# Optimization experiments

Hardware: AMD Instinct MI355X
Metric: run time of the kernel (lower is better)

## Reference

```python
import jax, jax.numpy as jnp
import numpy as np

N, E, C_IN, HID, K, NLAYERS = 1024, 2048, 4, 192, 5, 4


def setup_inputs() -> dict:
    key = jax.random.key(0)
    ks = jax.random.split(key, 24)
    s = 0.05
    x = jax.random.normal(ks[0], (N, C_IN), jnp.float32)
    src = jax.random.randint(ks[1], (E,), 0, N, dtype=jnp.int32)
    off = jax.random.randint(ks[2], (E,), 1, N, dtype=jnp.int32)
    dst = (src + off) % N  # guarantees no self-loops (ChebConv removes them)
    edge_index = jnp.stack([src, dst])  # [2, E] int32
    edge_attr = jax.random.normal(ks[3], (E, C_IN), jnp.float32)
    batch = jnp.zeros((N,), jnp.int32)  # unused by forward, kept for signature fidelity
    inp = {
        'x': x, 'edge_index': edge_index, 'edge_attr': edge_attr, 'batch': batch,
        # ChebConv(4, 192, K=5): K weight mats + bias
        'cheb_w': jax.random.normal(ks[4], (K, C_IN, HID), jnp.float32) * s,
        'cheb_b': jnp.zeros((HID,), jnp.float32),
        # edge encoder Linear(4, 192)
        'eenc_w': jax.random.normal(ks[5], (C_IN, HID), jnp.float32) * s,
        'eenc_b': jnp.zeros((HID,), jnp.float32),
        # 4 NNConv layers, each with MapE2NxN edge MLP (192->192->192*192),
        # root linear (192x192, no bias) and conv bias
        'nn1_w': jax.random.normal(ks[6], (NLAYERS, HID, HID), jnp.float32) * s,
        'nn1_b': jnp.zeros((NLAYERS, HID), jnp.float32),
        'nn2_w': jax.random.normal(ks[7], (NLAYERS, HID, HID * HID), jnp.float32) * (s / 8.0),
        'nn2_b': jnp.zeros((NLAYERS, HID * HID), jnp.float32),
        'root_w': jax.random.normal(ks[8], (NLAYERS, HID, HID), jnp.float32) * s,
        'conv_b': jnp.zeros((NLAYERS, HID), jnp.float32),
        # LayerNorm per DeepGCNLayer
        'ln_g': jnp.ones((NLAYERS, HID), jnp.float32),
        'ln_b': jnp.zeros((NLAYERS, HID), jnp.float32),
        # final Linear(192, 2)
        'out_w': jax.random.normal(ks[9], (HID, 2), jnp.float32) * s,
        'out_b': jnp.zeros((2,), jnp.float32),
    }
    return inp


def _layernorm(v, g, b):
    mu = jnp.mean(v, axis=-1, keepdims=True)
    var = jnp.mean(jnp.square(v - mu), axis=-1, keepdims=True)
    return (v - mu) * jax.lax.rsqrt(var + 1e-5) * g + b


def reference(x, edge_index, edge_attr, batch, cheb_w, cheb_b, eenc_w, eenc_b,
              nn1_w, nn1_b, nn2_w, nn2_b, root_w, conv_b, ln_g, ln_b, out_w, out_b):
    n = x.shape[0]
    src, dst = edge_index[0], edge_index[1]

    # ---- ChebConv (sym norm, lambda_max=2.0) => L_hat = -D^{-1/2} A D^{-1/2} ----
    deg = jax.ops.segment_sum(jnp.ones_like(src, dtype=x.dtype), src, num_segments=n)
    dinv = jnp.where(deg > 0, 1.0 / jnp.sqrt(jnp.maximum(deg, 1.0)), 0.0)
    wnorm = -dinv[src] * dinv[dst]  # [E]

    def lap(v):  # y = L_hat @ v : gather -> weight -> scatter-add
        return jax.ops.segment_sum(wnorm[:, None] * v[src], dst, num_segments=n)

    Tx0 = x
    out = Tx0 @ cheb_w[0]
    Tx1 = lap(Tx0)
    out = out + Tx1 @ cheb_w[1]
    for k in range(2, K):  # Chebyshev recurrence
        Tx2 = 2.0 * lap(Tx1) - Tx0
        out = out + Tx2 @ cheb_w[k]
        Tx0, Tx1 = Tx1, Tx2
    h = out + cheb_b  # [N, HID]

    # ---- edge encoder ----
    ea = edge_attr @ eenc_w + eenc_b  # [E, HID]

    # ---- NNConv: per-edge MLP-generated weight, gather->edge-GEMM->scatter ----
    def nnconv(v, i):
        theta = (ea @ nn1_w[i] + nn1_b[i]) @ nn2_w[i] + nn2_b[i]  # [E, HID*HID]
        theta = theta.reshape(E, HID, HID)
        msg = jnp.einsum('ei,eio->eo', v[src], theta)  # per-edge matvec
        agg = jax.ops.segment_sum(msg, dst, num_segments=n)  # aggr='add'
        return agg + v @ root_w[i] + conv_b[i]

    # layers[0].conv applied directly (no pre-norm/act)
    h = nnconv(h, 0)
    # layers[1:4] are DeepGCNLayer res+: x + conv(dropout(act(norm(x))))
    for i in range(1, NLAYERS):
        z = jax.nn.relu(_layernorm(h, ln_g[i], ln_b[i]))
        h = h + nnconv(z, i)
    # final: act(layers[0].norm(x)), dropout (eval=identity), linear
    h = jax.nn.relu(_layernorm(h, ln_g[0], ln_b[0]))
    return h @ out_w + out_b  # [N, 2]
```

## Files before the change

### kernel.cpp

```cpp
#include <hip/hip_runtime.h>
#include <stdint.h>

typedef _Float16 half8 __attribute__((ext_vector_type(8)));
typedef float f32x4 __attribute__((ext_vector_type(4)));

typedef const __attribute__((address_space(1))) void* gptr_t;
typedef __attribute__((address_space(3))) void* lptr_t;
static __device__ __forceinline__ void gll16(const void* g, void* l) {
  __builtin_amdgcn_global_load_lds((gptr_t)(unsigned long long)g,
                                   (lptr_t)(unsigned int)(unsigned long long)l,
                                   16, 0, 0);
}

__global__ __launch_bounds__(256)
void k_pb(const float* __restrict__ nn2_w, const float* __restrict__ nn2_b,
          const float* __restrict__ eenc_w, const float* __restrict__ eenc_b,
          const float* __restrict__ nn1_w, const float* __restrict__ nn1_b,
          const float* __restrict__ root_w, _Float16* __restrict__ Btl,
          const float* __restrict__ x, const int* __restrict__ ei,
          float* __restrict__ Tx, int* __restrict__ rowptr, int* __restrict__ eord) {
  __shared__ __align__(16) float smem[33728];
  int t = threadIdx.x;
  if (blockIdx.x >= 36) {
    if (blockIdx.x == 36) {
      if (blockIdx.y == 0) {
        float* cur = smem;
        float* yv = smem + 4096;
        float* deg = yv;
        for (int i = t; i < 1024; i += 256) deg[i] = 0.f;
        __syncthreads();
        for (int e = t; e < 2048; e += 256) atomicAdd(&deg[ei[e]], 1.f);
        __syncthreads();
        float wn[8];
#pragma unroll
        for (int i = 0; i < 8; ++i) {
          int e = t + 256 * i;
          int s = ei[e], d = ei[2048 + e];
          float ds = deg[s], dd = deg[d];
          float a = ds > 0.f ? 1.f / sqrtf(fmaxf(ds, 1.f)) : 0.f;
          float bb = dd > 0.f ? 1.f / sqrtf(fmaxf(dd, 1.f)) : 0.f;
          wn[i] = -a * bb;
        }
        __syncthreads();
        float4 prev[4];
#pragma unroll
        for (int q = 0; q < 4; ++q) {
          int i = t + 256 * q;
          float4 xv = ((const float4*)x)[i];
          ((float4*)cur)[i] = xv;
          ((float4*)Tx)[i] = xv;
        }
        __syncthreads();
        for (int rec = 0; rec < 4; ++rec) {
          for (int i = t; i < 4096; i += 256) yv[i] = 0.f;
          __syncthreads();
#pragma unroll
          for (int i = 0; i < 8; ++i) {
            int e = t + 256 * i;
            int s = ei[e], d = ei[2048 + e];
            float wv = wn[i];
#pragma unroll
            for (int c = 0; c < 4; ++c) atomicAdd(&yv[d * 4 + c], wv * cur[s * 4 + c]);
          }
          __syncthreads();
          float a = rec ? 2.f : 1.f;
#pragma unroll
          for (int q = 0; q < 4; ++q) {
            int i = t + 256 * q;
            float4 y4 = ((float4*)yv)[i];
            float4 c4 = ((float4*)cur)[i];
            float4 n4;
            n4.x = a * y4.x - (rec ? prev[q].x : 0.f);
            n4.y = a * y4.y - (rec ? prev[q].y : 0.f);
            n4.z = a * y4.z - (rec ? prev[q].z : 0.f);
            n4.w = a * y4.w - (rec ? prev[q].w : 0.f);
            prev[q] = c4;
            ((float4*)cur)[i] = n4;
            ((float4*)(Tx + (rec + 1) * 4096))[i] = n4;
          }
          __syncthreads();
        }
      } else if (blockIdx.y == 1) {
        int* cnt = (int*)smem;
        int* rp  = (int*)smem + 1024;
        int* wtot = (int*)smem + 2048;
        int lane = t & 63, wv = t >> 6;
        for (int i = t; i < 1024; i += 256) cnt[i] = 0;
        __syncthreads();
        for (int e = t; e < 2048; e += 256) atomicAdd(&cnt[ei[2048 + e]], 1);
        __syncthreads();
        int c0 = cnt[t * 4], c1 = cnt[t * 4 + 1], c2 = cnt[t * 4 + 2], c3 = cnt[t * 4 + 3];
        int s = c0 + c1 + c2 + c3;
        int inc = s;
#pragma unroll
        for (int off = 1; off < 64; off <<= 1) {
          int u = __shfl_up(inc, off);
          if (lane >= off) inc += u;
        }
        if (lane == 63) wtot[wv] = inc;
        __syncthreads();
        int woff = 0;
#pragma unroll
        for (int j = 0; j < 4; ++j) if (j < wv) woff += wtot[j];
        int excl = woff + inc - s;
        int4 r4; r4.x = excl; r4.y = excl + c0; r4.z = excl + c0 + c1; r4.w = excl + c0 + c1 + c2;
        *(int4*)(rowptr + t * 4) = r4;
        if (t == 0) rowptr[1024] = 2048;
        rp[t * 4] = r4.x; rp[t * 4 + 1] = r4.y; rp[t * 4 + 2] = r4.z; rp[t * 4 + 3] = r4.w;
        __syncthreads();
        for (int e = t; e < 2048; e += 256) {
          int d = ei[2048 + e];
          int slot = atomicAdd(&rp[d], 1);
          eord[slot] = e;
        }
      }
      return;
    }
    int l = blockIdx.y;
    for (int idx = t; idx < 36864; idx += 256) {
      float v = root_w[(size_t)l * 36864 + idx];
      int i = idx / 192, o = idx - i * 192;
      Btl[(size_t)l * 221184 + (i >> 3) * 9216 + (size_t)(960 + o) * 8 + (i & 7)] = (_Float16)v;
    }
    return;
  }
  int w = t >> 6, lane = t & 63;
  int l = blockIdx.y;
  int wcol = blockIdx.x * 1024 + w * 256;
  const float* W2l = nn2_w + (size_t)l * 7077888;
  char* ldsbase = (char*)smem + w * 32768;
  f32x4 nb4 = *(const f32x4*)(nn2_b + (size_t)l * 36864 + wcol + 4 * lane);

#define ISSUE(tile)                                                             \
  {                                                                             \
    _Pragma("unroll")                                                           \
    for (int r = 0; r < 4; ++r) {                                               \
      int row = (tile) * 4 + r;                                                 \
      gll16((const char*)(W2l + (size_t)row * 36864 + wcol) + lane * 16,        \
            ldsbase + ((tile) & 7) * 4096 + r * 1024 + lane * 16);              \
    }                                                                           \
  }

  ISSUE(0); ISSUE(1); ISSUE(2); ISSUE(3); ISSUE(4); ISSUE(5); ISSUE(6);
  if (t < 192) {
    float a0 = 0.f, a1 = 0.f, a2 = 0.f, a3 = 0.f, a4 = 0.f;
    const float* nw = nn1_w + (size_t)l * 36864 + t;
    for (int k = 0; k < 192; ++k) {
      float nv = nw[(size_t)k * 192];
      a0 += eenc_w[k] * nv;
      a1 += eenc_w[192 + k] * nv;
      a2 += eenc_w[384 + k] * nv;
      a3 += eenc_w[576 + k] * nv;
      a4 += eenc_b[k] * nv;
    }
    smem[32768 + t] = a0; smem[32960 + t] = a1; smem[33152 + t] = a2;
    smem[33344 + t] = a3; smem[33536 + t] = a4 + nn1_b[l * 192 + t];
  }
  __syncthreads();

  f32x4 a[5] = {};
  const float* Ms = smem + 32768;
  for (int tile = 0; tile < 48; ++tile) {
    if (tile < 41) ISSUE(tile + 7);
    if (tile < 41)       asm volatile("s_waitcnt vmcnt(28)" ::: "memory");
    else if (tile == 41) asm volatile("s_waitcnt vmcnt(24)" ::: "memory");
    else if (tile == 42) asm volatile("s_waitcnt vmcnt(20)" ::: "memory");
    else if (tile == 43) asm volatile("s_waitcnt vmcnt(16)" ::: "memory");
    else if (tile == 44) asm volatile("s_waitcnt vmcnt(12)" ::: "memory");
    else if (tile == 45) asm volatile("s_waitcnt vmcnt(8)" ::: "memory");
    else if (tile == 46) asm volatile("s_waitcnt vmcnt(4)" ::: "memory");
    else                 asm volatile("s_waitcnt vmcnt(0)" ::: "memory");
    const float* wb = (const float*)(ldsbase) + (tile & 7) * 1024;
    const float* Mt = Ms + tile * 4;
#pragma unroll
    for (int r = 0; r < 4; ++r) {
      f32x4 wv = *(const f32x4*)(wb + r * 256 + 4 * lane);
#pragma unroll
      for (int c = 0; c < 5; ++c) a[c] += Mt[c * 192 + r] * wv;
    }
  }
#undef ISSUE
  a[4] += nb4;
#pragma unroll
  for (int cc = 0; cc < 4; ++cc) {
    int col = wcol + 4 * lane + cc;
    int i = col / 192, o = col - i * 192;
    _Float16* B0 = Btl + (size_t)l * 221184 + (i >> 3) * 9216 + (i & 7);
#pragma unroll
    for (int c = 0; c < 5; ++c)
      B0[(size_t)(c * 192 + o) * 8] = (_Float16)a[c][cc];
  }
}

__global__ __launch_bounds__(256)
void k_y(const _Float16* __restrict__ z16, const _Float16* __restrict__ Btl,
         float* __restrict__ Y, const float* __restrict__ Tx,
         const float* __restrict__ cheb_w, const float* __restrict__ cheb_b, int layer) {
  __shared__ __align__(16) _Float16 Als[12288];
  int t = threadIdx.x;
  int w = t >> 6, lane = t & 63, l15 = lane & 15, q4 = lane >> 4;
  int e0 = blockIdx.x * 64, cb = blockIdx.y;
  if (layer == 0) {
#pragma unroll
    for (int it = 0; it < 6; ++it) {
      int u = it * 256 + t;
      int row = u & 63, ck = u >> 6;
      int n = e0 + row;
      float tv[5][4];
#pragma unroll
      for (int k = 0; k < 5; ++k) {
        float4 t4 = ((const float4*)(Tx + k * 4096))[n];
        tv[k][0] = t4.x; tv[k][1] = t4.y; tv[k][2] = t4.z; tv[k][3] = t4.w;
      }
      union { _Float16 h[8]; uint4 v; } u8;
#pragma unroll
      for (int j = 0; j < 8; ++j) {
        int o = ck * 8 + j;
        float acc = cheb_b[o];
#pragma unroll
        for (int k = 0; k < 5; ++k)
#pragma unroll
          for (int c = 0; c < 4; ++c)
            acc += tv[k][c] * cheb_w[(k * 4 + c) * 192 + o];
        u8.h[j] = (_Float16)acc;
      }
      *(uint4*)(Als + (size_t)u * 8) = u8.v;
    }
    __syncthreads();
  }
  const _Float16* Bt = Btl + (size_t)layer * 221184;
  const _Float16* ap = z16 + (((size_t)q4 * 1024) + e0 + w * 16 + l15) * 8;
  const _Float16* bp = Bt + (((size_t)q4 * 1152) + cb * 192 + l15) * 8;
  f32x4 acc[12] = {};
#pragma unroll
  for (int ks = 0; ks < 6; ++ks) {
    half8 av;
    if (layer == 0)
      av = *(const half8*)(Als + (((size_t)(ks * 4 + q4) * 64) + w * 16 + l15) * 8);
    else
      av = *(const half8*)(ap + (size_t)ks * 4 * 1024 * 8);
#pragma unroll
    for (int nt = 0; nt < 12; ++nt) {
      half8 bv = *(const half8*)(bp + (size_t)ks * 4 * 1152 * 8 + nt * 16 * 8);
      acc[nt] = __builtin_amdgcn_mfma_f32_16x16x32_f16(av, bv, acc[nt], 0, 0, 0);
    }
  }
#pragma unroll
  for (int nt = 0; nt < 12; ++nt) {
    int col = cb * 192 + nt * 16 + l15;
#pragma unroll
    for (int r = 0; r < 4; ++r) {
      int row = e0 + w * 16 + q4 * 4 + r;
      Y[(size_t)row * 1152 + col] = acc[nt][r];
    }
  }
}

__global__ __launch_bounds__(256)
void k_gn(const int* __restrict__ ei, const float* __restrict__ eattr,
          const int* __restrict__ rowptr, const int* __restrict__ eord,
          const float* __restrict__ Y, const float* __restrict__ hp,
          const float* __restrict__ cbv, const float* __restrict__ gg,
          const float* __restrict__ bb, float* __restrict__ ho,
          _Float16* __restrict__ zo, const float* __restrict__ out_w,
          const float* __restrict__ out_b, float* __restrict__ outp, int l) {
  int t = threadIdx.x, w = t >> 6, lane = t & 63;
  int n = blockIdx.x * 4 + w;
  int o0 = lane, o1 = lane + 64, o2 = lane + 128;
  float v0 = 0.f, v1 = 0.f, v2 = 0.f;
  int beg = rowptr[n], end = rowptr[n + 1];
  for (int idx = beg; idx < end; ++idx) {
    int e = eord[idx];
    int s = ei[e];
    float4 u = ((const float4*)eattr)[e];
    const float* yr = Y + (size_t)s * 1152;
    v0 += yr[o0] * u.x + yr[192 + o0] * u.y + yr[384 + o0] * u.z + yr[576 + o0] * u.w + yr[768 + o0];
    v1 += yr[o1] * u.x + yr[192 + o1] * u.y + yr[384 + o1] * u.z + yr[576 + o1] * u.w + yr[768 + o1];
    v2 += yr[o2] * u.x + yr[192 + o2] * u.y + yr[384 + o2] * u.z + yr[576 + o2] * u.w + yr[768 + o2];
  }
  const float* yn = Y + (size_t)n * 1152 + 960;
  v0 += yn[o0] + cbv[o0]; v1 += yn[o1] + cbv[o1]; v2 += yn[o2] + cbv[o2];
  if (l > 0) {
    v0 += hp[n * 192 + o0]; v1 += hp[n * 192 + o1]; v2 += hp[n * 192 + o2];
  }
  if (l < 3) {
    ho[n * 192 + o0] = v0; ho[n * 192 + o1] = v1; ho[n * 192 + o2] = v2;
  }
  float s1 = v0 + v1 + v2, s2 = v0 * v0 + v1 * v1 + v2 * v2;
#pragma unroll
  for (int off = 32; off >= 1; off >>= 1) {
    s1 += __shfl_xor(s1, off);
    s2 += __shfl_xor(s2, off);
  }
  float mu = s1 * (1.f / 192.f);
  float var = s2 * (1.f / 192.f) - mu * mu;
  float rcp = rsqrtf(var + 1e-5f);
  float z0v = fmaxf((v0 - mu) * rcp * gg[o0] + bb[o0], 0.f);
  float z1v = fmaxf((v1 - mu) * rcp * gg[o1] + bb[o1], 0.f);
  float z2v = fmaxf((v2 - mu) * rcp * gg[o2] + bb[o2], 0.f);
  if (l < 3) {
    zo[((size_t)(o0 >> 3) * 1024 + n) * 8 + (o0 & 7)] = (_Float16)z0v;
    zo[((size_t)(o1 >> 3) * 1024 + n) * 8 + (o1 & 7)] = (_Float16)z1v;
    zo[((size_t)(o2 >> 3) * 1024 + n) * 8 + (o2 & 7)] = (_Float16)z2v;
  } else {
    float a0 = z0v * out_w[o0 * 2] + z1v * out_w[o1 * 2] + z2v * out_w[o2 * 2];
    float a1 = z0v * out_w[o0 * 2 + 1] + z1v * out_w[o1 * 2 + 1] + z2v * out_w[o2 * 2 + 1];
#pragma unroll
    for (int off = 32; off >= 1; off >>= 1) {
      a0 += __shfl_xor(a0, off);
      a1 += __shfl_xor(a1, off);
    }
    if (lane == 0) {
      outp[n * 2] = a0 + out_b[0];
      outp[n * 2 + 1] = a1 + out_b[1];
    }
  }
}

extern "C" void kernel_launch(void* const* d_in, const int* in_sizes, int n_in,
                              void* d_out, int out_size, void* d_ws, size_t ws_size,
                              hipStream_t stream) {
  const float* x      = (const float*)d_in[0];
  const int*   ei     = (const int*)  d_in[1];
  const float* eattr  = (const float*)d_in[2];
  const float* cheb_w = (const float*)d_in[4];
  const float* cheb_b = (const float*)d_in[5];
  const float* eenc_w = (const float*)d_in[6];
  const float* eenc_b = (const float*)d_in[7];
  const float* nn1_w  = (const float*)d_in[8];
  const float* nn1_b  = (const float*)d_in[9];
  const float* nn2_w  = (const float*)d_in[10];
  const float* nn2_b  = (const float*)d_in[11];
  const float* root_w = (const float*)d_in[12];
  const float* conv_b = (const float*)d_in[13];
  const float* ln_g   = (const float*)d_in[14];
  const float* ln_bb  = (const float*)d_in[15];
  const float* out_w  = (const float*)d_in[16];
  const float* out_b  = (const float*)d_in[17];
  float* outp = (float*)d_out;
  (void)in_sizes; (void)n_in; (void)out_size; (void)ws_size;

  char* p = (char*)d_ws;
  _Float16* Btl = (_Float16*)p; p += (size_t)4 * 221184 * 2;
  float* Tx     = (float*)p;    p += 5 * 4096 * 4;
  float* Y      = (float*)p;    p += (size_t)1024 * 1152 * 4;
  float* hA     = (float*)p;    p += 196608 * 4;
  float* hB     = (float*)p;    p += 196608 * 4;
  _Float16* zA  = (_Float16*)p; p += 196608 * 2;
  _Float16* zB  = (_Float16*)p; p += 196608 * 2;
  int* rowptr   = (int*)p;      p += 1056 * 4;
  int* eord     = (int*)p;      p += 2048 * 4;

  k_pb<<<dim3(38, 4), 256, 0, stream>>>(nn2_w, nn2_b, eenc_w, eenc_b, nn1_w, nn1_b,
                                        root_w, Btl, x, ei, Tx, rowptr, eord);

  const _Float16* zin[4] = {zA, zA, zB, zA};
  _Float16* zout[4] = {zA, zB, zA, zA};
  float* hout[4] = {hA, hB, hA, hA};
  const float* hres[4] = {hA, hA, hB, hA};
  for (int l = 0; l < 4; ++l) {
    k_y<<<dim3(16, 6), 256, 0, stream>>>(zin[l], Btl, Y, Tx, cheb_w, cheb_b, l);
    k_gn<<<256, 256, 0, stream>>>(ei, eattr, rowptr, eord, Y, hres[l],
                                  conv_b + (size_t)l * 192,
                                  ln_g + (size_t)((l == 3) ? 0 : (l + 1)) * 192,
                                  ln_bb + (size_t)((l == 3) ? 0 : (l + 1)) * 192,
                                  hout[l], zout[l], out_w, out_b, outp, l);
  }
}
```

Baseline: 287.1 us.

## Split nn2 weight-folding reduction over K across blocks with separate reduce kernel

The per-layer folding of nn2_w (a 192x36864 fp32 stream per layer) is restructured. The old version used 36 column blocks per layer, each streaming all 192 rows through an LDS pipeline. The new version splits the K dimension into 4 chunks via blockIdx.z, giving 192 streaming blocks. Each thread keeps 15 register accumulators and uses plain global vector loads, and a new k_stage kernel sums the fp32 partials, adds the bias and writes the fp16 B tiles. This raises parallelism for the bandwidth-bound weight read, which is about 113 MB. In exchange it adds a partial buffer write and read of about 5.9 MB plus an extra launch, and it drops the explicit global-to-LDS prefetch.

```diff
diff --git a/kernel.cpp b/kernel.cpp
--- a/kernel.cpp
+++ b/kernel.cpp
@@ -4,144 +4,122 @@
 typedef _Float16 half8 __attribute__((ext_vector_type(8)));
 typedef float f32x4 __attribute__((ext_vector_type(4)));
 
-typedef const __attribute__((address_space(1))) void* gptr_t;
-typedef __attribute__((address_space(3))) void* lptr_t;
-static __device__ __forceinline__ void gll16(const void* g, void* l) {
-  __builtin_amdgcn_global_load_lds((gptr_t)(unsigned long long)g,
-                                   (lptr_t)(unsigned int)(unsigned long long)l,
-                                   16, 0, 0);
-}
-
 __global__ __launch_bounds__(256)
-void k_pb(const float* __restrict__ nn2_w, const float* __restrict__ nn2_b,
-          const float* __restrict__ eenc_w, const float* __restrict__ eenc_b,
-          const float* __restrict__ nn1_w, const float* __restrict__ nn1_b,
-          const float* __restrict__ root_w, _Float16* __restrict__ Btl,
+void k_pb(const float* __restrict__ nn2_w, const float* __restrict__ eenc_w,
+          const float* __restrict__ eenc_b, const float* __restrict__ nn1_w,
+          const float* __restrict__ nn1_b, const float* __restrict__ root_w,
+          float* __restrict__ Ppart, _Float16* __restrict__ Btl,
           const float* __restrict__ x, const int* __restrict__ ei,
           float* __restrict__ Tx, int* __restrict__ rowptr, int* __restrict__ eord) {
-  __shared__ __align__(16) float smem[33728];
+  __shared__ __align__(16) float smem[8192];
   int t = threadIdx.x;
-  if (blockIdx.x >= 36) {
-    if (blockIdx.x == 36) {
-      if (blockIdx.y == 0) {
-        float* cur = smem;
-        float* yv = smem + 4096;
-        float* deg = yv;
-        for (int i = t; i < 1024; i += 256) deg[i] = 0.f;
+  if (blockIdx.x == 12) {
+    if (blockIdx.z != 0) return;
+    if (blockIdx.y == 0) {
+      float* cur = smem;
+      float* yv = smem + 4096;
+      float* deg = yv;
+      for (int i = t; i < 1024; i += 256) deg[i] = 0.f;
+      __syncthreads();
+      for (int e = t; e < 2048; e += 256) atomicAdd(&deg[ei[e]], 1.f);
+      __syncthreads();
+      float wn[8];
+#pragma unroll
+      for (int i = 0; i < 8; ++i) {
+        int e = t + 256 * i;
+        int s = ei[e], d = ei[2048 + e];
+        float ds = deg[s], dd = deg[d];
+        float a = ds > 0.f ? 1.f / sqrtf(fmaxf(ds, 1.f)) : 0.f;
+        float bb = dd > 0.f ? 1.f / sqrtf(fmaxf(dd, 1.f)) : 0.f;
+        wn[i] = -a * bb;
+      }
+      __syncthreads();
+      float4 prev[4];
+#pragma unroll
+      for (int q = 0; q < 4; ++q) {
+        int i = t + 256 * q;
+        float4 xv = ((const float4*)x)[i];
+        ((float4*)cur)[i] = xv;
+        ((float4*)Tx)[i] = xv;
+      }
+      __syncthreads();
+      for (int rec = 0; rec < 4; ++rec) {
+        for (int i = t; i < 4096; i += 256) yv[i] = 0.f;
         __syncthreads();
-        for (int e = t; e < 2048; e += 256) atomicAdd(&deg[ei[e]], 1.f);
-        __syncthreads();
-        float wn[8];
 #pragma unroll
         for (int i = 0; i < 8; ++i) {
           int e = t + 256 * i;
           int s = ei[e], d = ei[2048 + e];
-          float ds = deg[s], dd = deg[d];
-          float a = ds > 0.f ? 1.f / sqrtf(fmaxf(ds, 1.f)) : 0.f;
-          float bb = dd > 0.f ? 1.f / sqrtf(fmaxf(dd, 1.f)) : 0.f;
-          wn[i] = -a * bb;
+          float wv = wn[i];
+#pragma unroll
+          for (int c = 0; c < 4; ++c) atomicAdd(&yv[d * 4 + c], wv * cur[s * 4 + c]);
         }
         __syncthreads();
-        float4 prev[4];
+        float a = rec ? 2.f : 1.f;
 #pragma unroll
         for (int q = 0; q < 4; ++q) {
           int i = t + 256 * q;
-          float4 xv = ((const float4*)x)[i];
-          ((float4*)cur)[i] = xv;
-          ((float4*)Tx)[i] = xv;
+          float4 y4 = ((float4*)yv)[i];
+          float4 c4 = ((float4*)cur)[i];
+          float4 n4;
+          n4.x = a * y4.x - (rec ? prev[q].x : 0.f);
+          n4.y = a * y4.y - (rec ? prev[q].y : 0.f);
+          n4.z = a * y4.z - (rec ? prev[q].z : 0.f);
+          n4.w = a * y4.w - (rec ? prev[q].w : 0.f);
+          prev[q] = c4;
+          ((float4*)cur)[i] = n4;
+          ((float4*)(Tx + (rec + 1) * 4096))[i] = n4;
         }
         __syncthreads();
-        for (int rec = 0; rec < 4; ++rec) {
-          for (int i = t; i < 4096; i += 256) yv[i] = 0.f;
-          __syncthreads();
-#pragma unroll
-          for (int i = 0; i < 8; ++i) {
-            int e = t + 256 * i;
-            int s = ei[e], d = ei[2048 + e];
-            float wv = wn[i];
-#pragma unroll
-            for (int c = 0; c < 4; ++c) atomicAdd(&yv[d * 4 + c], wv * cur[s * 4 + c]);
-          }
-          __syncthreads();
-          float a = rec ? 2.f : 1.f;
-#pragma unroll
-          for (int q = 0; q < 4; ++q) {
-            int i = t + 256 * q;
-            float4 y4 = ((float4*)yv)[i];
-            float4 c4 = ((float4*)cur)[i];
-            float4 n4;
-            n4.x = a * y4.x - (rec ? prev[q].x : 0.f);
-            n4.y = a * y4.y - (rec ? prev[q].y : 0.f);
-            n4.z = a * y4.z - (rec ? prev[q].z : 0.f);
-            n4.w = a * y4.w - (rec ? prev[q].w : 0.f);
-            prev[q] = c4;
-            ((float4*)cur)[i] = n4;
-            ((float4*)(Tx + (rec + 1) * 4096))[i] = n4;
-          }
-          __syncthreads();
+      }
+    } else if (blockIdx.y == 1) {
+      int* cnt = (int*)smem;
+      int* rp  = (int*)smem + 1024;
+      int* wtot = (int*)smem + 2048;
+      int lane = t & 63, wv = t >> 6;
+      for (int i = t; i < 1024; i += 256) cnt[i] = 0;
+      __syncthreads();
+      for (int e = t; e < 2048; e += 256) atomicAdd(&cnt[ei[2048 + e]], 1);
+      __syncthreads();
+      int c0 = cnt[t * 4], c1 = cnt[t * 4 + 1], c2 = cnt[t * 4 + 2], c3 = cnt[t * 4 + 3];
+      int s = c0 + c1 + c2 + c3;
+      int inc = s;
+#pragma unroll
+      for (int off = 1; off < 64; off <<= 1) {
+        int u = __shfl_up(inc, off);
+        if (lane >= off) inc += u;
+      }
+      if (lane == 63) wtot[wv] = inc;
+      __syncthreads();
+      int woff = 0;
+#pragma unroll
+      for (int j = 0; j < 4; ++j) if (j < wv) woff += wtot[j];
+      int excl = woff + inc - s;
+      int4 r4; r4.x = excl; r4.y = excl + c0; r4.z = excl + c0 + c1; r4.w = excl + c0 + c1 + c2;
+      *(int4*)(rowptr + t * 4) = r4;
+      if (t == 0) rowptr[1024] = 2048;
+      rp[t * 4] = r4.x; rp[t * 4 + 1] = r4.y; rp[t * 4 + 2] = r4.z; rp[t * 4 + 3] = r4.w;
+      __syncthreads();
+      for (int e = t; e < 2048; e += 256) {
+        int d = ei[2048 + e];
+        int slot = atomicAdd(&rp[d], 1);
+        eord[slot] = e;
+      }
+    } else {
+      int lbase = (blockIdx.y - 2) * 2;
+#pragma unroll
+      for (int rep = 0; rep < 2; ++rep) {
+        int l = lbase + rep;
+        for (int idx = t; idx < 36864; idx += 256) {
+          float v = root_w[(size_t)l * 36864 + idx];
+          int i = idx / 192, o = idx - i * 192;
+          Btl[(size_t)l * 221184 + (i >> 3) * 9216 + (size_t)(960 + o) * 8 + (i & 7)] = (_Float16)v;
         }
-      } else if (blockIdx.y == 1) {
-        int* cnt = (int*)smem;
-        int* rp  = (int*)smem + 1024;
-        int* wtot = (int*)smem + 2048;
-        int lane = t & 63, wv = t >> 6;
-        for (int i = t; i < 1024; i += 256) cnt[i] = 0;
-        __syncthreads();
-        for (int e = t; e < 2048; e += 256) atomicAdd(&cnt[ei[2048 + e]], 1);
-        __syncthreads();
-        int c0 = cnt[t * 4], c1 = cnt[t * 4 + 1], c2 = cnt[t * 4 + 2], c3 = cnt[t * 4 + 3];
-        int s = c0 + c1 + c2 + c3;
-        int inc = s;
-#pragma unroll
-        for (int off = 1; off < 64; off <<= 1) {
-          int u = __shfl_up(inc, off);
-          if (lane >= off) inc += u;
-        }
-        if (lane == 63) wtot[wv] = inc;
-        __syncthreads();
-        int woff = 0;
-#pragma unroll
-        for (int j = 0; j < 4; ++j) if (j < wv) woff += wtot[j];
-        int excl = woff + inc - s;
-        int4 r4; r4.x = excl; r4.y = excl + c0; r4.z = excl + c0 + c1; r4.w = excl + c0 + c1 + c2;
-        *(int4*)(rowptr + t * 4) = r4;
-        if (t == 0) rowptr[1024] = 2048;
-        rp[t * 4] = r4.x; rp[t * 4 + 1] = r4.y; rp[t * 4 + 2] = r4.z; rp[t * 4 + 3] = r4.w;
-        __syncthreads();
-        for (int e = t; e < 2048; e += 256) {
-          int d = ei[2048 + e];
-          int slot = atomicAdd(&rp[d], 1);
-          eord[slot] = e;
-        }
-      }
-      return;
-    }
-    int l = blockIdx.y;
-    for (int idx = t; idx < 36864; idx += 256) {
-      float v = root_w[(size_t)l * 36864 + idx];
-      int i = idx / 192, o = idx - i * 192;
-      Btl[(size_t)l * 221184 + (i >> 3) * 9216 + (size_t)(960 + o) * 8 + (i & 7)] = (_Float16)v;
+      }
     }
     return;
   }
-  int w = t >> 6, lane = t & 63;
-  int l = blockIdx.y;
-  int wcol = blockIdx.x * 1024 + w * 256;
-  const float* W2l = nn2_w + (size_t)l * 7077888;
-  char* ldsbase = (char*)smem + w * 32768;
-  f32x4 nb4 = *(const f32x4*)(nn2_b + (size_t)l * 36864 + wcol + 4 * lane);
-
-#define ISSUE(tile)                                                             \
-  {                                                                             \
-    _Pragma("unroll")                                                           \
-    for (int r = 0; r < 4; ++r) {                                               \
-      int row = (tile) * 4 + r;                                                 \
-      gll16((const char*)(W2l + (size_t)row * 36864 + wcol) + lane * 16,        \
-            ldsbase + ((tile) & 7) * 4096 + r * 1024 + lane * 16);              \
-    }                                                                           \
-  }
-
-  ISSUE(0); ISSUE(1); ISSUE(2); ISSUE(3); ISSUE(4); ISSUE(5); ISSUE(6);
+  int l = blockIdx.y, kq = blockIdx.z;
   if (t < 192) {
     float a0 = 0.f, a1 = 0.f, a2 = 0.f, a3 = 0.f, a4 = 0.f;
     const float* nw = nn1_w + (size_t)l * 36864 + t;
@@ -153,42 +131,65 @@
       a3 += eenc_w[576 + k] * nv;
       a4 += eenc_b[k] * nv;
     }
-    smem[32768 + t] = a0; smem[32960 + t] = a1; smem[33152 + t] = a2;
-    smem[33344 + t] = a3; smem[33536 + t] = a4 + nn1_b[l * 192 + t];
+    smem[t] = a0; smem[192 + t] = a1; smem[384 + t] = a2;
+    smem[576 + t] = a3; smem[768 + t] = a4 + nn1_b[l * 192 + t];
   }
   __syncthreads();
-
-  f32x4 a[5] = {};
-  const float* Ms = smem + 32768;
-  for (int tile = 0; tile < 48; ++tile) {
-    if (tile < 41) ISSUE(tile + 7);
-    if (tile < 41)       asm volatile("s_waitcnt vmcnt(28)" ::: "memory");
-    else if (tile == 41) asm volatile("s_waitcnt vmcnt(24)" ::: "memory");
-    else if (tile == 42) asm volatile("s_waitcnt vmcnt(20)" ::: "memory");
-    else if (tile == 43) asm volatile("s_waitcnt vmcnt(16)" ::: "memory");
-    else if (tile == 44) asm volatile("s_waitcnt vmcnt(12)" ::: "memory");
-    else if (tile == 45) asm volatile("s_waitcnt vmcnt(8)" ::: "memory");
-    else if (tile == 46) asm volatile("s_waitcnt vmcnt(4)" ::: "memory");
-    else                 asm volatile("s_waitcnt vmcnt(0)" ::: "memory");
-    const float* wb = (const float*)(ldsbase) + (tile & 7) * 1024;
-    const float* Mt = Ms + tile * 4;
-#pragma unroll
-    for (int r = 0; r < 4; ++r) {
-      f32x4 wv = *(const f32x4*)(wb + r * 256 + 4 * lane);
-#pragma unroll
-      for (int c = 0; c < 5; ++c) a[c] += Mt[c * 192 + r] * wv;
-    }
-  }
-#undef ISSUE
-  a[4] += nb4;
-#pragma unroll
-  for (int cc = 0; cc < 4; ++cc) {
-    int col = wcol + 4 * lane + cc;
-    int i = col / 192, o = col - i * 192;
-    _Float16* B0 = Btl + (size_t)l * 221184 + (i >> 3) * 9216 + (i & 7);
-#pragma unroll
-    for (int c = 0; c < 5; ++c)
-      B0[(size_t)(c * 192 + o) * 8] = (_Float16)a[c][cc];
+  const float* Wp = nn2_w + (size_t)l * 7077888 + (size_t)(kq * 48) * 36864
+                    + blockIdx.x * 3072 + t * 4;
+  const float* Ms = smem;
+  int k0 = kq * 48;
+  f32x4 acc0 = {}, acc1 = {}, acc2 = {}, acc3 = {}, acc4 = {};
+  f32x4 acc0b = {}, acc1b = {}, acc2b = {}, acc3b = {}, acc4b = {};
+  f32x4 acc0c = {}, acc1c = {}, acc2c = {}, acc3c = {}, acc4c = {};
+#pragma unroll 4
+  for (int r = 0; r < 48; ++r) {
+    const float* rp = Wp + (size_t)r * 36864;
+    f32x4 w0 = *(const f32x4*)(rp);
+    f32x4 w1 = *(const f32x4*)(rp + 1024);
+    f32x4 w2 = *(const f32x4*)(rp + 2048);
+    int k = k0 + r;
+    float m0 = Ms[k], m1 = Ms[192 + k], m2 = Ms[384 + k], m3 = Ms[576 + k], m4 = Ms[768 + k];
+    acc0 += m0 * w0; acc0b += m0 * w1; acc0c += m0 * w2;
+    acc1 += m1 * w0; acc1b += m1 * w1; acc1c += m1 * w2;
+    acc2 += m2 * w0; acc2b += m2 * w1; acc2c += m2 * w2;
+    acc3 += m3 * w0; acc3b += m3 * w1; acc3c += m3 * w2;
+    acc4 += m4 * w0; acc4b += m4 * w1; acc4c += m4 * w2;
+  }
+  float* Pp = Ppart + ((size_t)(kq * 4 + l) * 5) * 36864 + blockIdx.x * 3072 + t * 4;
+  *(f32x4*)(Pp) = acc0;               *(f32x4*)(Pp + 1024) = acc0b;        *(f32x4*)(Pp + 2048) = acc0c;
+  *(f32x4*)(Pp + 36864) = acc1;       *(f32x4*)(Pp + 36864 + 1024) = acc1b; *(f32x4*)(Pp + 36864 + 2048) = acc1c;
+  *(f32x4*)(Pp + 2 * 36864) = acc2;   *(f32x4*)(Pp + 2 * 36864 + 1024) = acc2b; *(f32x4*)(Pp + 2 * 36864 + 2048) = acc2c;
+  *(f32x4*)(Pp + 3 * 36864) = acc3;   *(f32x4*)(Pp + 3 * 36864 + 1024) = acc3b; *(f32x4*)(Pp + 3 * 36864 + 2048) = acc3c;
+  *(f32x4*)(Pp + 4 * 36864) = acc4;   *(f32x4*)(Pp + 4 * 36864 + 1024) = acc4b; *(f32x4*)(Pp + 4 * 36864 + 2048) = acc4c;
+}
+
+__global__ __launch_bounds__(256)
+void k_stage(const float* __restrict__ Ppart, const float* __restrict__ nn2_b,
+             _Float16* __restrict__ Btl) {
+  int t = threadIdx.x, l = blockIdx.y;
+  _Float16* base = Btl + (size_t)l * 221184;
+#pragma unroll
+  for (int q = 0; q < 4; ++q) {
+    int j = blockIdx.x * 1024 + q * 256 + t;
+    float s0 = 0.f, s1 = 0.f, s2 = 0.f, s3 = 0.f, s4 = 0.f;
+#pragma unroll
+    for (int kq = 0; kq < 4; ++kq) {
+      const float* Pp = Ppart + ((size_t)(kq * 4 + l) * 5) * 36864 + j;
+      s0 += Pp[0];
+      s1 += Pp[36864];
+      s2 += Pp[2 * 36864];
+      s3 += Pp[3 * 36864];
+      s4 += Pp[4 * 36864];
+    }
+    s4 += nn2_b[(size_t)l * 36864 + j];
+    int i = j / 192, o = j - i * 192;
+    _Float16* B0 = base + (i >> 3) * 9216 + (i & 7);
+    B0[(size_t)(0 * 192 + o) * 8] = (_Float16)s0;
+    B0[(size_t)(1 * 192 + o) * 8] = (_Float16)s1;
+    B0[(size_t)(2 * 192 + o) * 8] = (_Float16)s2;
+    B0[(size_t)(3 * 192 + o) * 8] = (_Float16)s3;
+    B0[(size_t)(4 * 192 + o) * 8] = (_Float16)s4;
   }
 }
 
@@ -342,6 +343,7 @@
 
   char* p = (char*)d_ws;
   _Float16* Btl = (_Float16*)p; p += (size_t)4 * 221184 * 2;
+  float* Ppart  = (float*)p;    p += (size_t)4 * 4 * 5 * 36864 * 4;
   float* Tx     = (float*)p;    p += 5 * 4096 * 4;
   float* Y      = (float*)p;    p += (size_t)1024 * 1152 * 4;
   float* hA     = (float*)p;    p += 196608 * 4;
@@ -351,8 +353,9 @@
   int* rowptr   = (int*)p;      p += 1056 * 4;
   int* eord     = (int*)p;      p += 2048 * 4;
 
-  k_pb<<<dim3(38, 4), 256, 0, stream>>>(nn2_w, nn2_b, eenc_w, eenc_b, nn1_w, nn1_b,
-                                        root_w, Btl, x, ei, Tx, rowptr, eord);
+  k_pb<<<dim3(13, 4, 4), 256, 0, stream>>>(nn2_w, eenc_w, eenc_b, nn1_w, nn1_b,
+                                           root_w, Ppart, Btl, x, ei, Tx, rowptr, eord);
+  k_stage<<<dim3(36, 4), 256, 0, stream>>>(Ppart, nn2_b, Btl);
 
   const _Float16* zin[4] = {zA, zA, zB, zA};
   _Float16* zout[4] = {zA, zB, zA, zA};
```

Measured after the change: 345.1 us. 1.2x slower.
